# Kernel optimization log

Measured on AMD Instinct MI355X. Metric: run time of the kernel, lower is better.

## Reference

```python
import jax, jax.numpy as jnp
import numpy as np

B, C, N, H = 4, 256, 4096, 4
DK = C // H


def _proj(x, w, b):
    # Conv1d with kernel size 1 == per-point linear: [B,C,N] x [O,C] -> [B,O,N]
    return jnp.einsum('oc,bcn->bon', w, x) + b[None, :, None]


def setup_inputs() -> dict:
    key = jax.random.key(0)
    ks = jax.random.split(key, 9)
    s = 1.0 / np.sqrt(C)
    return {
        'x': jax.random.normal(ks[0], (B, C, N), jnp.float32),
        'wq': jax.random.normal(ks[1], (C, C), jnp.float32) * s,
        'bq': jax.random.normal(ks[2], (C,), jnp.float32) * 0.01,
        'wk': jax.random.normal(ks[3], (C, C), jnp.float32) * s,
        'bk': jax.random.normal(ks[4], (C,), jnp.float32) * 0.01,
        'wv': jax.random.normal(ks[5], (C, C), jnp.float32) * s,
        'bv': jax.random.normal(ks[6], (C,), jnp.float32) * 0.01,
        'wp': jax.random.normal(ks[7], (C, C), jnp.float32) * s,
        'bp': jax.random.normal(ks[8], (C,), jnp.float32) * 0.01,
    }


def reference(x, wq, bq, wk, bk, wv, bv, wp, bp):
    b, c, n = x.shape
    q = _proj(x, wq, bq).reshape(b, H, DK, n)
    k = _proj(x, wk, bk).reshape(b, H, DK, n)
    v = _proj(x, wv, bv).reshape(b, H, DK, n)
    scale = 1.0 / jnp.sqrt(jnp.asarray(DK, x.dtype))
    # scores over point pairs: [B,H,N,N]
    scores = jnp.einsum('bhdn,bhdm->bhnm', q, k) * scale
    attn = jax.nn.softmax(scores, axis=-1)
    out = jnp.einsum('bhnm,bhdm->bhdn', attn, v)  # [B,H,DK,N]
    out = out.reshape(b, c, n)
    out = _proj(out, wp, bp)
    return out + x
```

## Files before the change

### kernel.cpp

```cpp
#include <hip/hip_runtime.h>


#define BDIM 4
#define CDIM 256
#define NDIM 4096
#define HDIM 4
#define DKDIM 64
#define NQ   (BDIM * HDIM * NDIM)
#define NSPLIT 4
#define KPERZ (NDIM / NSPLIT)
#define QSCALE 0.18033688011112042f

typedef __bf16 bf16x8 __attribute__((ext_vector_type(8)));
typedef float f32x4 __attribute__((ext_vector_type(4)));
typedef short s16x4 __attribute__((ext_vector_type(4)));
typedef unsigned short u16;
typedef unsigned int u32;

__device__ __forceinline__ u16 f2bf(float f) {
  union { __bf16 h; u16 s; } u; u.h = (__bf16)f; return u.s;
}
__device__ __forceinline__ float bf2f(u16 v) {
  union { u32 u; float f; } x; x.u = (u32)v << 16; return x.f;
}
__device__ __forceinline__ u32 pk2(float a, float b) {
  return (u32)f2bf(a) | ((u32)f2bf(b) << 16);
}

__global__ __launch_bounds__(256) void xt_kernel(
    const float* __restrict__ x, u16* __restrict__ xT)
{
  const int b = blockIdx.z, c0 = blockIdx.y * 64, n0 = blockIdx.x * 64;
  __shared__ __align__(16) float T[64][68];
  const int t = threadIdx.x;
  {
    const int cr = t >> 4, nc = (t & 15) * 4;
    #pragma unroll
    for (int ci = 0; ci < 4; ++ci) {
      const float4 v = *(const float4*)&x[((size_t)(b * CDIM + c0 + cr + ci * 16)) * NDIM + n0 + nc];
      *(float4*)&T[cr + ci * 16][nc] = v;
    }
  }
  __syncthreads();
  {
    const int n = t >> 2, g = t & 3;
    union { u16 u[16]; uint4 v[2]; } pk;
    #pragma unroll
    for (int u_ = 0; u_ < 16; ++u_) pk.u[u_] = f2bf(T[g * 16 + u_][n]);
    uint4* dst = (uint4*)&xT[((size_t)(b * NDIM + n0 + n)) * CDIM + c0 + g * 16];
    dst[0] = pk.v[0]; dst[1] = pk.v[1];
  }
}

__global__ __launch_bounds__(256, 4) void qkv_kernel(
    const u16* __restrict__ xT,
    const float* __restrict__ wq, const float* __restrict__ bq,
    const float* __restrict__ wk, const float* __restrict__ bk,
    const float* __restrict__ wv, const float* __restrict__ bv,
    u16* __restrict__ qT, u16* __restrict__ kT, u16* __restrict__ vB)
{
  const int b = blockIdx.z;
  const int p = blockIdx.y >> 1;
  const int o0 = (blockIdx.y & 1) * 128;
  const int n0 = blockIdx.x * 64;
  const float* wsel = (p == 0) ? wq : (p == 1) ? wk : wv;
  const float* bsel = (p == 0) ? bq : (p == 1) ? bk : bv;
  const float wscale = (p == 0) ? QSCALE : 1.0f;

  __shared__ __align__(16) u16 XTs[64][40];
  __shared__ __align__(16) u16 Ws[128][40];
  const int t = threadIdx.x, lane = t & 63, w = t >> 6;
  const int qd = lane >> 4, lm = lane & 15;
  const int sr = t >> 2, sg = (t & 3) * 8;
  const int r2 = t >> 1, g2 = (t & 1) * 16;

  const u16* xsrc = xT + ((size_t)(b * NDIM + n0 + sr)) * CDIM + sg;
  const float* wsrc = wsel + (size_t)(o0 + r2) * CDIM + g2;

  f32x4 acc[4][2];
  #pragma unroll
  for (int nt = 0; nt < 4; ++nt)
    #pragma unroll
    for (int j = 0; j < 2; ++j) acc[nt][j] = (f32x4){0.f, 0.f, 0.f, 0.f};

  for (int cs = 0; cs < 8; ++cs) {
    __syncthreads();
    *(uint4*)&XTs[sr][sg] = *(const uint4*)(xsrc + cs * 32);
    {
      const float4 w0 = *(const float4*)(wsrc + cs * 32);
      const float4 w1 = *(const float4*)(wsrc + cs * 32 + 4);
      const float4 w2 = *(const float4*)(wsrc + cs * 32 + 8);
      const float4 w3 = *(const float4*)(wsrc + cs * 32 + 12);
      union { u32 p[8]; uint4 v[2]; } pw;
      pw.p[0] = pk2(w0.x * wscale, w0.y * wscale);
      pw.p[1] = pk2(w0.z * wscale, w0.w * wscale);
      pw.p[2] = pk2(w1.x * wscale, w1.y * wscale);
      pw.p[3] = pk2(w1.z * wscale, w1.w * wscale);
      pw.p[4] = pk2(w2.x * wscale, w2.y * wscale);
      pw.p[5] = pk2(w2.z * wscale, w2.w * wscale);
      pw.p[6] = pk2(w3.x * wscale, w3.y * wscale);
      pw.p[7] = pk2(w3.z * wscale, w3.w * wscale);
      *(uint4*)&Ws[r2][g2]     = pw.v[0];
      *(uint4*)&Ws[r2][g2 + 8] = pw.v[1];
    }
    __syncthreads();
    bf16x8 xf[4], wf[2];
    #pragma unroll
    for (int nt = 0; nt < 4; ++nt) xf[nt] = *(const bf16x8*)&XTs[16 * nt + lm][qd * 8];
    #pragma unroll
    for (int j = 0; j < 2; ++j) wf[j] = *(const bf16x8*)&Ws[32 * w + 16 * j + lm][qd * 8];
    #pragma unroll
    for (int nt = 0; nt < 4; ++nt)
      #pragma unroll
      for (int j = 0; j < 2; ++j) {
        if (p < 2)
          acc[nt][j] = __builtin_amdgcn_mfma_f32_16x16x32_bf16(xf[nt], wf[j], acc[nt][j], 0, 0, 0);
        else
          acc[nt][j] = __builtin_amdgcn_mfma_f32_16x16x32_bf16(wf[j], xf[nt], acc[nt][j], 0, 0, 0);
      }
  }

  if (p < 2) {
    u16* out = (p == 0) ? qT : kT;
    #pragma unroll
    for (int j = 0; j < 2; ++j) {
      const int og = o0 + 32 * w + 16 * j + lm;
      const float bv2 = bsel[og] * wscale;
      #pragma unroll
      for (int nt = 0; nt < 4; ++nt)
        #pragma unroll
        for (int r = 0; r < 4; ++r) {
          const int n = n0 + 16 * nt + 4 * qd + r;
          out[((size_t)(b * NDIM + n)) * CDIM + og] = f2bf(acc[nt][j][r] + bv2);
        }
    }
  } else {
    #pragma unroll
    for (int j = 0; j < 2; ++j) {
      const float4 b4 = *(const float4*)&bsel[o0 + 32 * w + 16 * j + 4 * qd];
      const float bvr[4] = {b4.x, b4.y, b4.z, b4.w};
      #pragma unroll
      for (int nt = 0; nt < 4; ++nt)
        #pragma unroll
        for (int r = 0; r < 4; ++r) {
          const int og = o0 + 32 * w + 16 * j + 4 * qd + r;
          const int n = n0 + 16 * nt + lm;
          vB[((size_t)(b * CDIM + og)) * NDIM + n] = f2bf(acc[nt][j][r] + bvr[r]);
        }
    }
  }
}

__global__ __launch_bounds__(256, 4) void attn_kernel(
    const u16* __restrict__ qT, const u16* __restrict__ kT,
    const u16* __restrict__ vB, u16* __restrict__ Opart,
    float* __restrict__ Lp)
{
  const int bh = blockIdx.y, b = bh >> 2, h = bh & 3;
  const int n0 = blockIdx.x * 128;
  const int z  = blockIdx.z;

  __shared__ __align__(16) u16 KV[2][64][72];

  const int t = threadIdx.x, lane = t & 63, w = t >> 6;
  const int qd = lane >> 4, lm = lane & 15;

  bf16x8 qf[2][2];
  {
    const u16* qbase = qT + ((size_t)(b * NDIM) + n0) * CDIM + h * 64;
    #pragma unroll
    for (int s = 0; s < 2; ++s)
      #pragma unroll
      for (int hh = 0; hh < 2; ++hh)
        qf[s][hh] = *(const bf16x8*)(qbase +
            (size_t)(16 * (2 * w + s) + lm) * CDIM + 32 * hh + qd * 8);
  }

  float l_i[2] = {0.f, 0.f};
  f32x4 oa[2][4];
  #pragma unroll
  for (int s = 0; s < 2; ++s)
    #pragma unroll
    for (int dt = 0; dt < 4; ++dt) oa[s][dt] = (f32x4){0.f, 0.f, 0.f, 0.f};

  const int sr = t >> 2, sg = (t & 3) * 16;
  const u16* kptr = kT + ((size_t)(b * NDIM) + z * KPERZ + sr) * CDIM + h * 64 + sg;
  const u16* vptr = vB + ((size_t)(b * CDIM) + h * 64 + sr) * NDIM + z * KPERZ + sg;

  {
    const uint4 ka0 = *(const uint4*)(kptr);
    const uint4 kb0 = *(const uint4*)(kptr + 8);
    const uint4 va0 = *(const uint4*)(vptr);
    const uint4 vv0 = *(const uint4*)(vptr + 8);
    kptr += (size_t)64 * CDIM;
    vptr += 64;
    uint4* kd = (uint4*)&KV[0][sr][sg]; kd[0] = ka0; kd[1] = kb0;
    uint4* vd = (uint4*)&KV[1][sr][sg]; vd[0] = va0; vd[1] = vv0;
  }

  uint4 ka, kb, va, vv;
  #pragma unroll 1
  for (int it = 0; it < KPERZ / 64; ++it) {
    const bool pf = (it + 1 < KPERZ / 64);
    if (pf) {
      ka = *(const uint4*)(kptr);
      kb = *(const uint4*)(kptr + 8);
      va = *(const uint4*)(vptr);
      vv = *(const uint4*)(vptr + 8);
      kptr += (size_t)64 * CDIM;
      vptr += 64;
    }
    __builtin_amdgcn_sched_barrier(0);
    __syncthreads();

    union { u16 u[4]; s16x4 v; } pk[2][4];
    float rs[2] = {0.f, 0.f};

    #pragma unroll
    for (int nt = 0; nt < 4; ++nt) {
      const bf16x8 kf0 = *(const bf16x8*)&KV[0][16 * nt + lm][qd * 8];
      const bf16x8 kf1 = *(const bf16x8*)&KV[0][16 * nt + lm][32 + qd * 8];
      #pragma unroll
      for (int s = 0; s < 2; ++s) {
        f32x4 zz = (f32x4){0.f, 0.f, 0.f, 0.f};
        __builtin_amdgcn_s_setprio(1);
        zz = __builtin_amdgcn_mfma_f32_16x16x32_bf16(kf0, qf[s][0], zz, 0, 0, 0);
        zz = __builtin_amdgcn_mfma_f32_16x16x32_bf16(kf1, qf[s][1], zz, 0, 0, 0);
        __builtin_amdgcn_s_setprio(0);
        #pragma unroll
        for (int r = 0; r < 4; ++r) {
          const float p = __builtin_amdgcn_exp2f(zz[r]);
          pk[s][nt].u[r] = f2bf(p);
          rs[s] += p;
        }
      }
    }
    l_i[0] += rs[0];
    l_i[1] += rs[1];

    #pragma unroll
    for (int c = 0; c < 4; ++c) {
      s16x4 av[4];
      #pragma unroll
      for (int dt = 0; dt < 4; ++dt)
        av[dt] = *(const s16x4*)&KV[1][16 * dt + lm][16 * c + 4 * qd];
      __builtin_amdgcn_s_setprio(1);
      #pragma unroll
      for (int dt = 0; dt < 4; ++dt) {
        oa[0][dt] = __builtin_amdgcn_mfma_f32_16x16x16bf16_1k(av[dt], pk[0][c].v, oa[0][dt], 0, 0, 0);
        oa[1][dt] = __builtin_amdgcn_mfma_f32_16x16x16bf16_1k(av[dt], pk[1][c].v, oa[1][dt], 0, 0, 0);
      }
      __builtin_amdgcn_s_setprio(0);
    }

    __syncthreads();
    if (pf) {
      uint4* kd = (uint4*)&KV[0][sr][sg]; kd[0] = ka; kd[1] = kb;
      uint4* vd = (uint4*)&KV[1][sr][sg]; vd[0] = va; vd[1] = vv;
    }
  }

  #pragma unroll
  for (int s = 0; s < 2; ++s) {
    l_i[s] += __shfl_xor(l_i[s], 16);
    l_i[s] += __shfl_xor(l_i[s], 32);
  }

  u16 (*Ot)[72] = (u16(*)[72])&KV[0][0][0];
  #pragma unroll
  for (int s = 0; s < 2; ++s) {
    const float inv = 1.0f / l_i[s];
    #pragma unroll
    for (int dt = 0; dt < 4; ++dt)
      #pragma unroll
      for (int r = 0; r < 4; ++r)
        Ot[16 * (2 * w + s) + lm][16 * dt + 4 * qd + r] = f2bf(oa[s][dt][r] * inv);
  }
  if (qd == 0) {
    const size_t lbase = ((size_t)z * (BDIM * HDIM) + bh) * NDIM;
    #pragma unroll
    for (int s = 0; s < 2; ++s)
      Lp[lbase + n0 + 16 * (2 * w + s) + lm] = l_i[s];
  }
  __syncthreads();
  {
    const int r = t >> 1, g = (t & 1) * 32;
    u16* dst = Opart + (((size_t)z * (BDIM * HDIM) + bh) * NDIM + n0 + r) * DKDIM + g;
    const uint4* srcp = (const uint4*)&Ot[r][g];
    uint4* d4 = (uint4*)dst;
    d4[0] = srcp[0]; d4[1] = srcp[1]; d4[2] = srcp[2]; d4[3] = srcp[3];
  }
}

__global__ __launch_bounds__(256, 4) void projout_kernel(
    const u16* __restrict__ Opart, const float* __restrict__ Lp,
    const float* __restrict__ wp, const float* __restrict__ bp,
    const float* __restrict__ res, float* __restrict__ out)
{
  const int b = blockIdx.z, o0 = blockIdx.y * 128, n0 = blockIdx.x * 64;
  __shared__ __align__(16) u16 XTs[64][40];
  __shared__ __align__(16) u16 Ws[128][40];
  const int t = threadIdx.x, lane = t & 63, w = t >> 6;
  const int qd = lane >> 4, lm = lane & 15;
  const int sr = t >> 2, sg = (t & 3) * 8;
  const int r2 = t >> 1, g2 = (t & 1) * 16;

  float wh[4][NSPLIT];
  #pragma unroll
  for (int hh = 0; hh < 4; ++hh) {
    const size_t i0 = ((size_t)(b * HDIM + hh)) * NDIM + n0 + sr;
    float l[NSPLIT], tot = 0.f;
    #pragma unroll
    for (int zz = 0; zz < NSPLIT; ++zz) { l[zz] = Lp[(size_t)zz * NQ + i0]; tot += l[zz]; }
    const float iv = 1.0f / tot;
    #pragma unroll
    for (int zz = 0; zz < NSPLIT; ++zz) wh[hh][zz] = l[zz] * iv;
  }

  const float* wsrc = wp + (size_t)(o0 + r2) * CDIM + g2;

  f32x4 acc[4][2];
  #pragma unroll
  for (int nt = 0; nt < 4; ++nt)
    #pragma unroll
    for (int j = 0; j < 2; ++j) acc[nt][j] = (f32x4){0.f, 0.f, 0.f, 0.f};

  for (int cs = 0; cs < 8; ++cs) {
    const int c0 = cs * 32;
    const int hh = c0 >> 6;
    const int dk = (c0 & 63) + sg;
    __syncthreads();
    {
      const size_t obase = (((size_t)(b * HDIM + hh)) * NDIM + n0 + sr) * DKDIM + dk;
      float v[8] = {0.f, 0.f, 0.f, 0.f, 0.f, 0.f, 0.f, 0.f};
      #pragma unroll
      for (int zz = 0; zz < NSPLIT; ++zz) {
        union { u16 u[8]; uint4 q; } a;
        a.q = *(const uint4*)(Opart + (size_t)zz * NQ * DKDIM + obase);
        const float wz = wh[hh][zz];
        #pragma unroll
        for (int j = 0; j < 8; ++j) v[j] = fmaf(wz, bf2f(a.u[j]), v[j]);
      }
      union { u16 u[8]; uint4 q; } ov;
      #pragma unroll
      for (int j = 0; j < 8; ++j) ov.u[j] = f2bf(v[j]);
      *(uint4*)&XTs[sr][sg] = ov.q;
      const float4 wv0 = *(const float4*)(wsrc + c0);
      const float4 wv1 = *(const float4*)(wsrc + c0 + 4);
      const float4 wv2 = *(const float4*)(wsrc + c0 + 8);
      const float4 wv3 = *(const float4*)(wsrc + c0 + 12);
      union { u32 p[8]; uint4 v[2]; } pw;
      pw.p[0] = pk2(wv0.x, wv0.y); pw.p[1] = pk2(wv0.z, wv0.w);
      pw.p[2] = pk2(wv1.x, wv1.y); pw.p[3] = pk2(wv1.z, wv1.w);
      pw.p[4] = pk2(wv2.x, wv2.y); pw.p[5] = pk2(wv2.z, wv2.w);
      pw.p[6] = pk2(wv3.x, wv3.y); pw.p[7] = pk2(wv3.z, wv3.w);
      *(uint4*)&Ws[r2][g2]     = pw.v[0];
      *(uint4*)&Ws[r2][g2 + 8] = pw.v[1];
    }
    __syncthreads();
    bf16x8 xf[4], wf[2];
    #pragma unroll
    for (int nt = 0; nt < 4; ++nt) xf[nt] = *(const bf16x8*)&XTs[16 * nt + lm][qd * 8];
    #pragma unroll
    for (int j = 0; j < 2; ++j) wf[j] = *(const bf16x8*)&Ws[32 * w + 16 * j + lm][qd * 8];
    #pragma unroll
    for (int nt = 0; nt < 4; ++nt)
      #pragma unroll
      for (int j = 0; j < 2; ++j)
        acc[nt][j] = __builtin_amdgcn_mfma_f32_16x16x32_bf16(wf[j], xf[nt], acc[nt][j], 0, 0, 0);
  }

  #pragma unroll
  for (int j = 0; j < 2; ++j) {
    const float4 b4 = *(const float4*)&bp[o0 + 32 * w + 16 * j + 4 * qd];
    const float bvr[4] = {b4.x, b4.y, b4.z, b4.w};
    #pragma unroll
    for (int nt = 0; nt < 4; ++nt)
      #pragma unroll
      for (int r = 0; r < 4; ++r) {
        const int og = o0 + 32 * w + 16 * j + 4 * qd + r;
        const int n = n0 + 16 * nt + lm;
        const size_t idx = ((size_t)(b * CDIM + og)) * NDIM + n;
        out[idx] = acc[nt][j][r] + bvr[r] + res[idx];
      }
  }
}

extern "C" void kernel_launch(void* const* d_in, const int* in_sizes, int n_in,
                              void* d_out, int out_size, void* d_ws, size_t ws_size,
                              hipStream_t stream)
{
  const float* x  = (const float*)d_in[0];
  const float* wq = (const float*)d_in[1];
  const float* bq = (const float*)d_in[2];
  const float* wk = (const float*)d_in[3];
  const float* bk = (const float*)d_in[4];
  const float* wv = (const float*)d_in[5];
  const float* bv = (const float*)d_in[6];
  const float* wp = (const float*)d_in[7];
  const float* bp = (const float*)d_in[8];
  float* out = (float*)d_out;

  const size_t sz = (size_t)BDIM * CDIM * NDIM;
  u16* xTb = (u16*)d_ws;
  u16* qTb = xTb + sz;
  u16* kTb = qTb + sz;
  u16* vBb = kTb + sz;
  u16* Opart = vBb + sz;
  float* Lp = (float*)(Opart + (size_t)NSPLIT * sz);

  const dim3 blk(256);
  xt_kernel<<<dim3(NDIM / 64, CDIM / 64, BDIM), blk, 0, stream>>>(x, xTb);
  qkv_kernel<<<dim3(NDIM / 64, 6, BDIM), blk, 0, stream>>>(
      xTb, wq, bq, wk, bk, wv, bv, qTb, kTb, vBb);
  attn_kernel<<<dim3(NDIM / 128, BDIM * HDIM, NSPLIT), blk, 0, stream>>>(
      qTb, kTb, vBb, Opart, Lp);
  projout_kernel<<<dim3(NDIM / 64, 2, BDIM), blk, 0, stream>>>(
      Opart, Lp, wp, bp, x, out);
}
```

Measured before the change: 212.5 us.

## Stream K/V tiles directly into swizzled double-buffered LDS via global_load_lds

The attention kernel now fetches K and V tiles with global_load_lds straight into a double-buffered LDS array instead of staging them through registers. The prefetch for the next tile is issued right after a single barrier per iteration. Rows use an XOR swizzle in place of padding to avoid bank conflicts, and the MFMA and LDS reads index through that swizzle. This frees the registers that held the prefetched tile and removes the second barrier per iteration, and the setprio hints are dropped. In exchange LDS use grows to 32KB per block, and correctness depends on the async LDS writes being complete before the barrier.

```diff
diff --git a/kernel.cpp b/kernel.cpp
--- a/kernel.cpp
+++ b/kernel.cpp
@@ -25,6 +25,11 @@
 }
 __device__ __forceinline__ u32 pk2(float a, float b) {
   return (u32)f2bf(a) | ((u32)f2bf(b) << 16);
+}
+__device__ __forceinline__ void gload16(const u16* g, u16* l) {
+  __builtin_amdgcn_global_load_lds(
+      (const __attribute__((address_space(1))) void*)g,
+      (__attribute__((address_space(3))) void*)l, 16, 0, 0);
 }
 
 __global__ __launch_bounds__(256) void xt_kernel(
@@ -160,10 +165,10 @@
   const int n0 = blockIdx.x * 128;
   const int z  = blockIdx.z;
 
-  __shared__ __align__(16) u16 KV[2][64][72];
+  __shared__ __align__(16) u16 KVlds[2][2][64][64];
 
   const int t = threadIdx.x, lane = t & 63, w = t >> 6;
-  const int qd = lane >> 4, lm = lane & 15;
+  const int qd = lane >> 4, lm = lane & 15, l7 = lm & 7;
 
   bf16x8 qf[2][2];
   {
@@ -183,50 +188,50 @@
     #pragma unroll
     for (int dt = 0; dt < 4; ++dt) oa[s][dt] = (f32x4){0.f, 0.f, 0.f, 0.f};
 
-  const int sr = t >> 2, sg = (t & 3) * 16;
-  const u16* kptr = kT + ((size_t)(b * NDIM) + z * KPERZ + sr) * CDIM + h * 64 + sg;
-  const u16* vptr = vB + ((size_t)(b * CDIM) + h * 64 + sr) * NDIM + z * KPERZ + sg;
+  const int srow = lane >> 3;
+  const int swz  = 8 * ((lane & 7) ^ srow);
+  const u16* kp0 = kT + ((size_t)(b * NDIM + z * KPERZ + 8 * w + srow)) * CDIM + h * 64 + swz;
+  const u16* kp1 = kp0 + (size_t)32 * CDIM;
+  const u16* vp0 = vB + ((size_t)(b * CDIM + h * 64 + 8 * w + srow)) * NDIM + z * KPERZ + swz;
+  const u16* vp1 = vp0 + (size_t)32 * NDIM;
 
   {
-    const uint4 ka0 = *(const uint4*)(kptr);
-    const uint4 kb0 = *(const uint4*)(kptr + 8);
-    const uint4 va0 = *(const uint4*)(vptr);
-    const uint4 vv0 = *(const uint4*)(vptr + 8);
-    kptr += (size_t)64 * CDIM;
-    vptr += 64;
-    uint4* kd = (uint4*)&KV[0][sr][sg]; kd[0] = ka0; kd[1] = kb0;
-    uint4* vd = (uint4*)&KV[1][sr][sg]; vd[0] = va0; vd[1] = vv0;
-  }
-
-  uint4 ka, kb, va, vv;
+    u16* kb = &KVlds[0][0][0][0];
+    u16* vb2 = &KVlds[0][1][0][0];
+    gload16(kp0, kb + w * 512);
+    gload16(kp1, kb + (4 + w) * 512);
+    gload16(vp0, vb2 + w * 512);
+    gload16(vp1, vb2 + (4 + w) * 512);
+  }
+
   #pragma unroll 1
   for (int it = 0; it < KPERZ / 64; ++it) {
-    const bool pf = (it + 1 < KPERZ / 64);
-    if (pf) {
-      ka = *(const uint4*)(kptr);
-      kb = *(const uint4*)(kptr + 8);
-      va = *(const uint4*)(vptr);
-      vv = *(const uint4*)(vptr + 8);
-      kptr += (size_t)64 * CDIM;
-      vptr += 64;
-    }
-    __builtin_amdgcn_sched_barrier(0);
     __syncthreads();
+    if (it + 1 < KPERZ / 64) {
+      const size_t ko = (size_t)(it + 1) * 64 * CDIM;
+      const int    vo = (it + 1) * 64;
+      u16* kb = &KVlds[(it + 1) & 1][0][0][0];
+      u16* vb2 = &KVlds[(it + 1) & 1][1][0][0];
+      gload16(kp0 + ko, kb + w * 512);
+      gload16(kp1 + ko, kb + (4 + w) * 512);
+      gload16(vp0 + vo, vb2 + w * 512);
+      gload16(vp1 + vo, vb2 + (4 + w) * 512);
+    }
+    const u16 (*Kt)[64] = KVlds[it & 1][0];
+    const u16 (*Vt)[64] = KVlds[it & 1][1];
 
     union { u16 u[4]; s16x4 v; } pk[2][4];
     float rs[2] = {0.f, 0.f};
 
     #pragma unroll
     for (int nt = 0; nt < 4; ++nt) {
-      const bf16x8 kf0 = *(const bf16x8*)&KV[0][16 * nt + lm][qd * 8];
-      const bf16x8 kf1 = *(const bf16x8*)&KV[0][16 * nt + lm][32 + qd * 8];
+      const bf16x8 kf0 = *(const bf16x8*)&Kt[16 * nt + lm][8 * (qd ^ l7)];
+      const bf16x8 kf1 = *(const bf16x8*)&Kt[16 * nt + lm][8 * ((4 + qd) ^ l7)];
       #pragma unroll
       for (int s = 0; s < 2; ++s) {
         f32x4 zz = (f32x4){0.f, 0.f, 0.f, 0.f};
-        __builtin_amdgcn_s_setprio(1);
         zz = __builtin_amdgcn_mfma_f32_16x16x32_bf16(kf0, qf[s][0], zz, 0, 0, 0);
         zz = __builtin_amdgcn_mfma_f32_16x16x32_bf16(kf1, qf[s][1], zz, 0, 0, 0);
-        __builtin_amdgcn_s_setprio(0);
         #pragma unroll
         for (int r = 0; r < 4; ++r) {
           const float p = __builtin_amdgcn_exp2f(zz[r]);
@@ -243,20 +248,12 @@
       s16x4 av[4];
       #pragma unroll
       for (int dt = 0; dt < 4; ++dt)
-        av[dt] = *(const s16x4*)&KV[1][16 * dt + lm][16 * c + 4 * qd];
-      __builtin_amdgcn_s_setprio(1);
+        av[dt] = *(const s16x4*)&Vt[16 * dt + lm][(16 * c + 4 * qd) ^ (8 * l7)];
       #pragma unroll
       for (int dt = 0; dt < 4; ++dt) {
         oa[0][dt] = __builtin_amdgcn_mfma_f32_16x16x16bf16_1k(av[dt], pk[0][c].v, oa[0][dt], 0, 0, 0);
         oa[1][dt] = __builtin_amdgcn_mfma_f32_16x16x16bf16_1k(av[dt], pk[1][c].v, oa[1][dt], 0, 0, 0);
       }
-      __builtin_amdgcn_s_setprio(0);
-    }
-
-    __syncthreads();
-    if (pf) {
-      uint4* kd = (uint4*)&KV[0][sr][sg]; kd[0] = ka; kd[1] = kb;
-      uint4* vd = (uint4*)&KV[1][sr][sg]; vd[0] = va; vd[1] = vv;
     }
   }
 
@@ -266,7 +263,8 @@
     l_i[s] += __shfl_xor(l_i[s], 32);
   }
 
-  u16 (*Ot)[72] = (u16(*)[72])&KV[0][0][0];
+  __syncthreads();
+  u16 (*Ot)[72] = (u16(*)[72])&KVlds[0][0][0][0];
   #pragma unroll
   for (int s = 0; s < 2; ++s) {
     const float inv = 1.0f / l_i[s];
```

Result: faster. 202.2 us (-4.8%).
